# Kernel optimization log

Hardware: AMD Instinct MI355X
Metric: run time of the kernel (lower is better)

The kernel has to match this reference:

```python
import jax, jax.numpy as jnp
import numpy as np
import math

NUM_HEADS = 8
DIM_EMBED = 640
DIM_CROSS = 768
DIM_HEAD = DIM_EMBED // NUM_HEADS


def setup_inputs() -> dict:
    key = jax.random.key(0)
    ks = jax.random.split(key, 10)
    B, SQ, SKV = 32, 1024, 77
    s_e = 1.0 / math.sqrt(DIM_EMBED)
    s_c = 1.0 / math.sqrt(DIM_CROSS)
    return {
        "x": jax.random.normal(ks[0], (B, SQ, DIM_EMBED), jnp.float32),
        "y": jax.random.normal(ks[1], (B, SKV, DIM_CROSS), jnp.float32),
        "Wq": jax.random.normal(ks[2], (DIM_EMBED, DIM_EMBED), jnp.float32) * s_e,
        "bq": jax.random.normal(ks[3], (DIM_EMBED,), jnp.float32) * 0.01,
        "Wk": jax.random.normal(ks[4], (DIM_CROSS, DIM_EMBED), jnp.float32) * s_c,
        "bk": jax.random.normal(ks[5], (DIM_EMBED,), jnp.float32) * 0.01,
        "Wv": jax.random.normal(ks[6], (DIM_CROSS, DIM_EMBED), jnp.float32) * s_c,
        "bv": jax.random.normal(ks[7], (DIM_EMBED,), jnp.float32) * 0.01,
        "Wo": jax.random.normal(ks[8], (DIM_EMBED, DIM_EMBED), jnp.float32) * s_e,
        "bo": jax.random.normal(ks[9], (DIM_EMBED,), jnp.float32) * 0.01,
    }


def reference(x, y, Wq, bq, Wk, bk, Wv, bv, Wo, bo):
    B, SQ, E = x.shape
    H, D = NUM_HEADS, DIM_HEAD
    q = x @ Wq + bq                      # [B, SQ, E]
    k = y @ Wk + bk                      # [B, SKV, E]
    v = y @ Wv + bv                      # [B, SKV, E]
    q = q.reshape(B, SQ, H, D)
    k = k.reshape(B, -1, H, D)
    v = v.reshape(B, -1, H, D)
    scores = jnp.einsum("bqhd,bkhd->bhqk", q, k) / math.sqrt(D)
    w = jax.nn.softmax(scores, axis=-1)
    out = jnp.einsum("bhqk,bkhd->bqhd", w, v).reshape(B, SQ, E)
    return out @ Wo + bo
```

## Files before the change

kernel.cpp:

```cpp
#include <hip/hip_runtime.h>
#include <hip/hip_bf16.h>

typedef __bf16 bf16x8 __attribute__((ext_vector_type(8)));
typedef float f32x4 __attribute__((ext_vector_type(4)));
typedef unsigned short us8 __attribute__((ext_vector_type(8)));
typedef unsigned int u32x4 __attribute__((ext_vector_type(4)));

#define E_ 640
#define CD_ 768
#define B_ 32
#define SQ_ 1024
#define SKV_ 77
#define H_ 8
#define DH_ 80

typedef __attribute__((address_space(3))) unsigned int as3_u32;
typedef __attribute__((address_space(1))) const unsigned int as1_u32;

__device__ __forceinline__ void gload16(const unsigned short* g, unsigned short* l) {
    __builtin_amdgcn_global_load_lds((as1_u32*)g, (as3_u32*)l, 16, 0, 0);
}

__device__ __forceinline__ float b2f(unsigned short u) {
    unsigned int x = ((unsigned int)u) << 16;
    return __builtin_bit_cast(float, x);
}
__device__ __forceinline__ unsigned short f2b(float f) {
    unsigned int x = __builtin_bit_cast(unsigned int, f);
    x += 0x7fffu + ((x >> 16) & 1u);
    return (unsigned short)(x >> 16);
}
__device__ __forceinline__ bf16x8 lv8(const unsigned short* p) {
    return __builtin_bit_cast(bf16x8, *reinterpret_cast<const us8*>(p));
}
__device__ __forceinline__ bf16x8 zero8() {
    us8 z = {0,0,0,0,0,0,0,0};
    return __builtin_bit_cast(bf16x8, z);
}
__device__ __forceinline__ bf16x8 cvtpk8(f32x4 lo, f32x4 hi) {
    unsigned int w0, w1, w2, w3;
    asm("v_cvt_pk_bf16_f32 %0, %1, %2" : "=v"(w0) : "v"(lo[0]), "v"(lo[1]));
    asm("v_cvt_pk_bf16_f32 %0, %1, %2" : "=v"(w1) : "v"(lo[2]), "v"(lo[3]));
    asm("v_cvt_pk_bf16_f32 %0, %1, %2" : "=v"(w2) : "v"(hi[0]), "v"(hi[1]));
    asm("v_cvt_pk_bf16_f32 %0, %1, %2" : "=v"(w3) : "v"(hi[2]), "v"(hi[3]));
    u32x4 w = {w0, w1, w2, w3};
    return __builtin_bit_cast(bf16x8, w);
}
__device__ __forceinline__ us8 cvt8(const float* s) {
    f32x4 f0 = *reinterpret_cast<const f32x4*>(s);
    f32x4 f1 = *reinterpret_cast<const f32x4*>(s + 4);
    return __builtin_bit_cast(us8, cvtpk8(f0, f1));
}

__device__ __forceinline__ void transpose_body(
    const float* __restrict__ in, unsigned short* __restrict__ out,
    int K, int N, int bx, int by, unsigned short (*t)[33])
{
    const int tx = threadIdx.x & 31, ty = threadIdx.x >> 5;
    const int n0 = bx * 32, k0 = by * 32;
#pragma unroll
    for (int i = 0; i < 4; ++i)
        t[ty + 8*i][tx] = f2b(in[(size_t)(k0 + ty + 8*i) * N + n0 + tx]);
    __syncthreads();
#pragma unroll
    for (int i = 0; i < 4; ++i)
        out[(size_t)(n0 + ty + 8*i) * K + k0 + tx] = t[tx][ty + 8*i];
}

__global__ __launch_bounds__(256) void fused_prep(
    const float* __restrict__ Wq, unsigned short* __restrict__ WqT,
    const float* __restrict__ Wo, unsigned short* __restrict__ WoT,
    const float* __restrict__ Wk, unsigned short* __restrict__ WkT,
    const float* __restrict__ Wv, unsigned short* __restrict__ WvT,
    const float* __restrict__ x, unsigned short* __restrict__ Xb)
{
    __shared__ unsigned short t[32][33];
    const int id = blockIdx.x;
    if (id < 800) {
        int z = id / 400, rem = id % 400;
        transpose_body(z ? Wo : Wq, z ? WoT : WqT, 640, 640, rem % 20, rem / 20, t);
    } else if (id < 1760) {
        int id2 = id - 800, z = id2 / 480, rem = id2 % 480;
        transpose_body(z ? Wv : Wk, z ? WvT : WkT, 768, 640, rem % 20, rem / 20, t);
    } else {
        long i = (long)(id - 1760) * 256 + threadIdx.x;
        const long stride = 2048L * 256;
        for (const long n8 = 2621440L; i < n8; i += stride)
            *reinterpret_cast<us8*>(Xb + i * 8) = cvt8(x + i * 8);
    }
}

template<int AMODE, bool CF32>
__device__ __forceinline__ void gemm_body(
    const void* __restrict__ Ap,
    const unsigned short* __restrict__ Wt,
    const float* __restrict__ bias,
    void* __restrict__ Cp,
    int M, int K, int ldc, int m0, int n0,
    unsigned short* smem)
{
    const int tid = threadIdx.x, lane = tid & 63, wave = tid >> 6;
    const int wr = (wave >> 1) << 6, wc = (wave & 1) << 6;
    const int l15 = lane & 15, l4 = lane >> 4;
    const int sgz = (tid >> 3) & 3;
    const int srd = (l15 >> 1) & 3;
    const int rdo = (l4 ^ srd) << 3;

    const unsigned short* gW0 = Wt + (size_t)(n0 + (tid >> 2)) * K + (((tid & 3) ^ sgz) << 3);
    const unsigned short* gW1 = Wt + (size_t)(n0 + (tid >> 2) + 64) * K + (((tid & 3) ^ sgz) << 3);

    const unsigned short* gA0; const unsigned short* gA1;
    const float* fA0; const float* fA1;
    int sw0, sw1;
    if constexpr (AMODE == 0) {
        gA0 = (const unsigned short*)Ap + (size_t)(m0 + (tid >> 2)) * K + (((tid & 3) ^ sgz) << 3);
        gA1 = (const unsigned short*)Ap + (size_t)(m0 + (tid >> 2) + 64) * K + (((tid & 3) ^ sgz) << 3);
    } else {
        int r0 = m0 + (tid >> 2); if (r0 >= M) r0 = M - 1;
        int r1 = r0 + 64; if (r1 >= M) r1 = M - 1;
        fA0 = (const float*)Ap + (size_t)r0 * K + (tid & 3) * 8;
        fA1 = (const float*)Ap + (size_t)r1 * K + (tid & 3) * 8;
        sw0 = ((tid & ~3) | ((tid & 3) ^ sgz)) * 8;
        sw1 = sw0 + 256 * 8;
    }

    f32x4 acc[4][4];
#pragma unroll
    for (int m = 0; m < 4; ++m)
#pragma unroll
        for (int n = 0; n < 4; ++n)
#pragma unroll
            for (int i = 0; i < 4; ++i) acc[m][n][i] = 0.f;

    auto STAGE = [&](int buf) {
        unsigned short* As = smem + buf * 8192;
        unsigned short* Ws = As + 4096;
        if constexpr (AMODE == 0) {
            gload16(gA0, As + tid * 8);
            gload16(gA1, As + (tid + 256) * 8);
            gA0 += 32; gA1 += 32;
        } else {
            *reinterpret_cast<us8*>(As + sw0) = cvt8(fA0);
            *reinterpret_cast<us8*>(As + sw1) = cvt8(fA1);
            fA0 += 32; fA1 += 32;
        }
        gload16(gW0, Ws + tid * 8);
        gload16(gW1, Ws + (tid + 256) * 8);
        gW0 += 32; gW1 += 32;
    };
    auto COMPUTE = [&](int buf) {
        const unsigned short* As = smem + buf * 8192;
        const unsigned short* Ws = As + 4096;
        bf16x8 a[4], b[4];
#pragma unroll
        for (int m = 0; m < 4; ++m)
            a[m] = lv8(&As[(wr + m * 16 + l15) * 32 + rdo]);
#pragma unroll
        for (int n = 0; n < 4; ++n)
            b[n] = lv8(&Ws[(wc + n * 16 + l15) * 32 + rdo]);
        __builtin_amdgcn_s_setprio(1);
#pragma unroll
        for (int m = 0; m < 4; ++m)
#pragma unroll
            for (int n = 0; n < 4; ++n)
                acc[m][n] = __builtin_amdgcn_mfma_f32_16x16x32_bf16(a[m], b[n], acc[m][n], 0, 0, 0);
        __builtin_amdgcn_s_setprio(0);
    };

    const int nk = K >> 5;
    STAGE(0);
    __syncthreads();
    for (int kt = 0; kt < nk - 2; kt += 2) {
        STAGE(1);
        COMPUTE(0);
        __syncthreads();
        STAGE(0);
        COMPUTE(1);
        __syncthreads();
    }
    STAGE(1);
    COMPUTE(0);
    __syncthreads();
    COMPUTE(1);

    float bs[4];
#pragma unroll
    for (int n = 0; n < 4; ++n) bs[n] = bias[n0 + wc + n * 16 + l15];

    if constexpr (CF32) {
        float* C = (float*)Cp;
        float* fs = (float*)smem;
#pragma unroll
        for (int p = 0; p < 2; ++p) {
            __syncthreads();
            if (wr == p * 64) {
#pragma unroll
                for (int m = 0; m < 4; ++m)
#pragma unroll
                    for (int n = 0; n < 4; ++n)
#pragma unroll
                        for (int i = 0; i < 4; ++i)
                            fs[(m * 16 + l4 * 4 + i) * 128 + wc + n * 16 + l15] =
                                acc[m][n][i] + bs[n];
            }
            __syncthreads();
#pragma unroll
            for (int r = 0; r < 8; ++r) {
                const int off = (r * 256 + tid) * 4;
                const int row = off >> 7, col = off & 127;
                const int grow = m0 + p * 64 + row;
                if (grow < M)
                    *reinterpret_cast<f32x4*>(&C[(size_t)grow * ldc + n0 + col]) =
                        *reinterpret_cast<const f32x4*>(&fs[off]);
            }
        }
    } else {
        unsigned short* C = (unsigned short*)Cp;
#pragma unroll
        for (int p = 0; p < 2; ++p) {
            __syncthreads();
            if (wr == p * 64) {
#pragma unroll
                for (int m = 0; m < 4; ++m)
#pragma unroll
                    for (int n = 0; n < 4; ++n)
#pragma unroll
                        for (int i = 0; i < 4; ++i)
                            smem[(m * 16 + l4 * 4 + i) * 128 + wc + n * 16 + l15] =
                                f2b(acc[m][n][i] + bs[n]);
            }
            __syncthreads();
#pragma unroll
            for (int r = 0; r < 4; ++r) {
                const int off = (r * 256 + tid) * 8;
                const int row = off >> 7, col = off & 127;
                const int grow = m0 + p * 64 + row;
                if (grow < M)
                    *reinterpret_cast<us8*>(&C[(size_t)grow * ldc + n0 + col]) =
                        *reinterpret_cast<us8*>(&smem[off]);
            }
        }
    }
}

__global__ __launch_bounds__(256) void gemm_o(
    const unsigned short* __restrict__ Ap, const unsigned short* __restrict__ Wt,
    const float* __restrict__ bias, float* __restrict__ Cp)
{
    __shared__ __align__(16) unsigned short smem[16384];
    const int orig = blockIdx.x;
    const int wgid = (orig & 7) * 160 + (orig >> 3);
    gemm_body<0, true>(Ap, Wt, bias, Cp, 32768, 640, 640,
                       (wgid / 5) * 128, (wgid % 5) * 128, smem);
}

__global__ __launch_bounds__(256) void fused_qkv(
    const unsigned short* __restrict__ Xb, const unsigned short* __restrict__ WqT,
    const float* __restrict__ bq, unsigned short* __restrict__ Qb,
    const float* __restrict__ y,
    const unsigned short* __restrict__ WkT, const float* __restrict__ bk2, unsigned short* __restrict__ Kb,
    const unsigned short* __restrict__ WvT, const float* __restrict__ bv2, unsigned short* __restrict__ Vb)
{
    __shared__ __align__(16) unsigned short smem[16384];
    const int id = blockIdx.x;
    if (id < 200) {
        int z = id / 100, rem = id % 100;
        int m0 = (rem / 5) * 128, n0 = (rem % 5) * 128;
        if (z == 0) gemm_body<1, false>(y, WkT, bk2, Kb, 2464, 768, 640, m0, n0, smem);
        else        gemm_body<1, false>(y, WvT, bv2, Vb, 2464, 768, 640, m0, n0, smem);
    } else {
        int orig = id - 200;
        int wgid = (orig & 7) * 160 + (orig >> 3);
        int m0 = (wgid / 5) * 128, n0 = (wgid % 5) * 128;
        gemm_body<0, false>(Xb, WqT, bq, Qb, 32768, 640, 640, m0, n0, smem);
    }
}

__global__ __launch_bounds__(256) void vtrans_kernel(
    const unsigned short* __restrict__ Vb, unsigned short* __restrict__ Vt)
{
    __shared__ unsigned short Vl[77 * 88 + 8];
    const int b = blockIdx.x, h = blockIdx.y;
    const int tid = threadIdx.x;
    for (int idx = tid; idx < 770; idx += 256) {
        int kv = idx / 10, seg = idx % 10;
        *reinterpret_cast<us8*>(&Vl[kv * 88 + seg * 8]) =
            *reinterpret_cast<const us8*>(&Vb[(size_t)(b * 77 + kv) * 640 + h * 80 + seg * 8]);
    }
    __syncthreads();
    unsigned short* out = Vt + (size_t)(b * 8 + h) * 6400;
    for (int idx = tid; idx < 800; idx += 256) {
        int d = idx / 10, seg = idx % 10;
        us8 v;
#pragma unroll
        for (int j = 0; j < 8; ++j) {
            int kv = seg * 8 + j;
            v[j] = (kv < 77) ? Vl[kv * 88 + d] : (unsigned short)0;
        }
        *reinterpret_cast<us8*>(&out[d * 80 + seg * 8]) = v;
    }
}

__global__ __launch_bounds__(128) void attn_kernel(
    const unsigned short* __restrict__ Q,
    const unsigned short* __restrict__ Kp,
    const unsigned short* __restrict__ Vt,
    unsigned short* __restrict__ Oa)
{
    __shared__ __align__(16) unsigned short smem[11272];
    const int tid = threadIdx.x, lane = tid & 63, wave = tid >> 6;
    const int l15 = lane & 15, l4 = lane >> 4;
    const int qb = blockIdx.x * 128, h = blockIdx.y, b = blockIdx.z;
    const size_t qrow0 = (size_t)b * SQ_ + qb + wave * 64;
    const size_t kbase = (size_t)b * SKV_ * E_ + h * DH_;
    const size_t vbase = (size_t)(b * 8 + h) * 6400;

    bf16x8 aq[3][4];
#pragma unroll
    for (int ks = 0; ks < 3; ++ks) {
        const int d = ks * 32 + l4 * 8;
#pragma unroll
        for (int m = 0; m < 4; ++m)
            aq[ks][m] = (d < 80) ? lv8(&Q[(qrow0 + m * 16 + l15) * E_ + h * DH_ + d]) : zero8();
    }

    f32x4 accS[4][5];
#pragma unroll
    for (int m = 0; m < 4; ++m)
#pragma unroll
        for (int n = 0; n < 5; ++n)
#pragma unroll
            for (int i = 0; i < 4; ++i) accS[m][n][i] = 0.f;

#pragma unroll
    for (int ks = 0; ks < 3; ++ks) {
        const int d = ks * 32 + l4 * 8;
        bf16x8 bk[5];
#pragma unroll
        for (int n = 0; n < 5; ++n) {
            const int kv = n * 16 + l15;
            bk[n] = (kv < SKV_ && d < 80) ? lv8(&Kp[kbase + (size_t)kv * E_ + d]) : zero8();
        }
        __builtin_amdgcn_s_setprio(1);
#pragma unroll
        for (int n = 0; n < 5; ++n)
#pragma unroll
            for (int m = 0; m < 4; ++m)
                accS[m][n] = __builtin_amdgcn_mfma_f32_16x16x32_bf16(aq[ks][m], bk[n], accS[m][n], 0, 0, 0);
        __builtin_amdgcn_s_setprio(0);
    }

    unsigned short* Pw = smem + wave * 5632;

    const float scale = 0.11180339887498949f;
    float rs[4][4];
#pragma unroll
    for (int m = 0; m < 4; ++m) {
#pragma unroll
        for (int i = 0; i < 4; ++i) {
            float mx = -1e30f;
#pragma unroll
            for (int n = 0; n < 5; ++n) {
                float s = accS[m][n][i] * scale;
                if (n == 4 && l15 >= 13) s = -1e30f;
                accS[m][n][i] = s;
                mx = fmaxf(mx, s);
            }
            mx = fmaxf(mx, __shfl_xor(mx, 1));
            mx = fmaxf(mx, __shfl_xor(mx, 2));
            mx = fmaxf(mx, __shfl_xor(mx, 4));
            mx = fmaxf(mx, __shfl_xor(mx, 8));
            float sum = 0.f;
            const int prow = m * 16 + l4 * 4 + i;
#pragma unroll
            for (int n = 0; n < 5; ++n) {
                float p = __expf(accS[m][n][i] - mx);
                sum += p;
                Pw[prow * 88 + n * 16 + l15] = f2b(p);
            }
            sum += __shfl_xor(sum, 1);
            sum += __shfl_xor(sum, 2);
            sum += __shfl_xor(sum, 4);
            sum += __shfl_xor(sum, 8);
            rs[m][i] = sum;
        }
    }

    f32x4 accO[4][5];
#pragma unroll
    for (int m = 0; m < 4; ++m)
#pragma unroll
        for (int n = 0; n < 5; ++n)
#pragma unroll
            for (int i = 0; i < 4; ++i) accO[m][n][i] = 0.f;

#pragma unroll
    for (int ks = 0; ks < 3; ++ks) {
        const int kv = ks * 32 + l4 * 8;
        bf16x8 ap[4], bv[5];
#pragma unroll
        for (int m = 0; m < 4; ++m)
            ap[m] = (ks < 2 || l4 < 2) ? lv8(&Pw[(m * 16 + l15) * 88 + ks * 32 + l4 * 8])
                                       : zero8();
#pragma unroll
        for (int n = 0; n < 5; ++n) {
            const int d = n * 16 + l15;
            bv[n] = (kv < 80) ? lv8(&Vt[vbase + (size_t)d * 80 + kv]) : zero8();
        }
        __builtin_amdgcn_s_setprio(1);
#pragma unroll
        for (int n = 0; n < 5; ++n)
#pragma unroll
            for (int m = 0; m < 4; ++m)
                accO[m][n] = __builtin_amdgcn_mfma_f32_16x16x32_bf16(ap[m], bv[n], accO[m][n], 0, 0, 0);
        __builtin_amdgcn_s_setprio(0);
    }

    __syncthreads();
#pragma unroll
    for (int m = 0; m < 4; ++m) {
#pragma unroll
        for (int i = 0; i < 4; ++i) {
            const float inv = 1.f / rs[m][i];
            const int rl = wave * 64 + m * 16 + l4 * 4 + i;
#pragma unroll
            for (int n = 0; n < 5; ++n)
                smem[rl * 80 + n * 16 + l15] = f2b(accO[m][n][i] * inv);
        }
    }
    __syncthreads();
    const size_t obase = (size_t)b * SQ_ + qb;
    for (int idx = tid; idx < 1280; idx += 128) {
        int row = idx / 10, seg = idx % 10;
        *reinterpret_cast<us8*>(&Oa[(obase + row) * E_ + h * DH_ + seg * 8]) =
            *reinterpret_cast<us8*>(&smem[row * 80 + seg * 8]);
    }
}

extern "C" void kernel_launch(void* const* d_in, const int* in_sizes, int n_in,
                              void* d_out, int out_size, void* d_ws, size_t ws_size,
                              hipStream_t stream) {
    const float* x  = (const float*)d_in[0];
    const float* y  = (const float*)d_in[1];
    const float* Wq = (const float*)d_in[2];
    const float* bq = (const float*)d_in[3];
    const float* Wk = (const float*)d_in[4];
    const float* bk = (const float*)d_in[5];
    const float* Wv = (const float*)d_in[6];
    const float* bv = (const float*)d_in[7];
    const float* Wo = (const float*)d_in[8];
    const float* bo = (const float*)d_in[9];
    float* out = (float*)d_out;

    char* ws = (char*)d_ws;
    unsigned short* WqT = (unsigned short*)(ws + 0);
    unsigned short* WkT = (unsigned short*)(ws + 819200);
    unsigned short* WvT = (unsigned short*)(ws + 1802240);
    unsigned short* WoT = (unsigned short*)(ws + 2785280);
    unsigned short* Qb  = (unsigned short*)(ws + 3604480);
    unsigned short* Kb  = (unsigned short*)(ws + 45547520);
    unsigned short* Vb  = (unsigned short*)(ws + 48701440);
    unsigned short* Xb  = (unsigned short*)(ws + 51855360);
    unsigned short* Vtb = (unsigned short*)(ws + 51855360);

    fused_prep<<<3808, 256, 0, stream>>>(Wq, WqT, Wo, WoT, Wk, WkT, Wv, WvT, x, Xb);
    fused_qkv<<<1480, 256, 0, stream>>>(Xb, WqT, bq, Qb, y, WkT, bk, Kb, WvT, bv, Vb);
    vtrans_kernel<<<dim3(32, 8), 256, 0, stream>>>(Vb, Vtb);
    attn_kernel<<<dim3(8, 8, 32), 128, 0, stream>>>(Qb, Kb, Vtb, Qb);
    gemm_o<<<1280, 256, 0, stream>>>(Qb, WoT, bo, out);
}
```

Baseline: 172.5 us.

## Rebalance kernel stages: fuse x conversion with K/V GEMMs and V transpose with Q GEMM

Moves the x-to-bf16 conversion out of the weight-prep kernel into the K/V projection kernel, and folds the standalone V transpose into the Q projection kernel as extra blocks. This cuts one kernel launch and lets the small K/V GEMM and V transpose work overlap with larger, bandwidth-bound work instead of running as separate, underfilled stages. Vt now gets its own workspace region instead of aliasing Xb, because Xb is still being read while the transpose runs.

```diff
diff --git a/kernel.cpp b/kernel.cpp
--- a/kernel.cpp
+++ b/kernel.cpp
@@ -71,22 +71,16 @@
     const float* __restrict__ Wq, unsigned short* __restrict__ WqT,
     const float* __restrict__ Wo, unsigned short* __restrict__ WoT,
     const float* __restrict__ Wk, unsigned short* __restrict__ WkT,
-    const float* __restrict__ Wv, unsigned short* __restrict__ WvT,
-    const float* __restrict__ x, unsigned short* __restrict__ Xb)
+    const float* __restrict__ Wv, unsigned short* __restrict__ WvT)
 {
     __shared__ unsigned short t[32][33];
     const int id = blockIdx.x;
     if (id < 800) {
         int z = id / 400, rem = id % 400;
         transpose_body(z ? Wo : Wq, z ? WoT : WqT, 640, 640, rem % 20, rem / 20, t);
-    } else if (id < 1760) {
+    } else {
         int id2 = id - 800, z = id2 / 480, rem = id2 % 480;
         transpose_body(z ? Wv : Wk, z ? WvT : WkT, 768, 640, rem % 20, rem / 20, t);
-    } else {
-        long i = (long)(id - 1760) * 256 + threadIdx.x;
-        const long stride = 2048L * 256;
-        for (const long n8 = 2621440L; i < n8; i += stride)
-            *reinterpret_cast<us8*>(Xb + i * 8) = cvt8(x + i * 8);
     }
 }
 
@@ -243,20 +237,8 @@
     }
 }
 
-__global__ __launch_bounds__(256) void gemm_o(
-    const unsigned short* __restrict__ Ap, const unsigned short* __restrict__ Wt,
-    const float* __restrict__ bias, float* __restrict__ Cp)
-{
-    __shared__ __align__(16) unsigned short smem[16384];
-    const int orig = blockIdx.x;
-    const int wgid = (orig & 7) * 160 + (orig >> 3);
-    gemm_body<0, true>(Ap, Wt, bias, Cp, 32768, 640, 640,
-                       (wgid / 5) * 128, (wgid % 5) * 128, smem);
-}
-
-__global__ __launch_bounds__(256) void fused_qkv(
-    const unsigned short* __restrict__ Xb, const unsigned short* __restrict__ WqT,
-    const float* __restrict__ bq, unsigned short* __restrict__ Qb,
+__global__ __launch_bounds__(256) void fused_cvt_kv(
+    const float* __restrict__ x, unsigned short* __restrict__ Xb,
     const float* __restrict__ y,
     const unsigned short* __restrict__ WkT, const float* __restrict__ bk2, unsigned short* __restrict__ Kb,
     const unsigned short* __restrict__ WvT, const float* __restrict__ bv2, unsigned short* __restrict__ Vb)
@@ -269,18 +251,17 @@
         if (z == 0) gemm_body<1, false>(y, WkT, bk2, Kb, 2464, 768, 640, m0, n0, smem);
         else        gemm_body<1, false>(y, WvT, bv2, Vb, 2464, 768, 640, m0, n0, smem);
     } else {
-        int orig = id - 200;
-        int wgid = (orig & 7) * 160 + (orig >> 3);
-        int m0 = (wgid / 5) * 128, n0 = (wgid % 5) * 128;
-        gemm_body<0, false>(Xb, WqT, bq, Qb, 32768, 640, 640, m0, n0, smem);
-    }
-}
-
-__global__ __launch_bounds__(256) void vtrans_kernel(
-    const unsigned short* __restrict__ Vb, unsigned short* __restrict__ Vt)
-{
-    __shared__ unsigned short Vl[77 * 88 + 8];
-    const int b = blockIdx.x, h = blockIdx.y;
+        long i = (long)(id - 200) * 256 + threadIdx.x;
+        const long stride = 2048L * 256;
+        for (const long n8 = 2621440L; i < n8; i += stride)
+            *reinterpret_cast<us8*>(Xb + i * 8) = cvt8(x + i * 8);
+    }
+}
+
+__device__ __forceinline__ void vtrans_body(
+    const unsigned short* __restrict__ Vb, unsigned short* __restrict__ Vt,
+    int b, int h, unsigned short* Vl)
+{
     const int tid = threadIdx.x;
     for (int idx = tid; idx < 770; idx += 256) {
         int kv = idx / 10, seg = idx % 10;
@@ -299,6 +280,34 @@
         }
         *reinterpret_cast<us8*>(&out[d * 80 + seg * 8]) = v;
     }
+}
+
+__global__ __launch_bounds__(256) void fused_q_vt(
+    const unsigned short* __restrict__ Xb, const unsigned short* __restrict__ WqT,
+    const float* __restrict__ bq, unsigned short* __restrict__ Qb,
+    const unsigned short* __restrict__ Vb, unsigned short* __restrict__ Vtb)
+{
+    __shared__ __align__(16) unsigned short smem[16384];
+    const int id = blockIdx.x;
+    if (id < 1280) {
+        int wgid = (id & 7) * 160 + (id >> 3);
+        int m0 = (wgid / 5) * 128, n0 = (wgid % 5) * 128;
+        gemm_body<0, false>(Xb, WqT, bq, Qb, 32768, 640, 640, m0, n0, smem);
+    } else {
+        int r = id - 1280;
+        vtrans_body(Vb, Vtb, r >> 3, r & 7, smem);
+    }
+}
+
+__global__ __launch_bounds__(256) void gemm_o(
+    const unsigned short* __restrict__ Ap, const unsigned short* __restrict__ Wt,
+    const float* __restrict__ bias, float* __restrict__ Cp)
+{
+    __shared__ __align__(16) unsigned short smem[16384];
+    const int orig = blockIdx.x;
+    const int wgid = (orig & 7) * 160 + (orig >> 3);
+    gemm_body<0, true>(Ap, Wt, bias, Cp, 32768, 640, 640,
+                       (wgid / 5) * 128, (wgid % 5) * 128, smem);
 }
 
 __global__ __launch_bounds__(128) void attn_kernel(
@@ -461,11 +470,11 @@
     unsigned short* Kb  = (unsigned short*)(ws + 45547520);
     unsigned short* Vb  = (unsigned short*)(ws + 48701440);
     unsigned short* Xb  = (unsigned short*)(ws + 51855360);
-    unsigned short* Vtb = (unsigned short*)(ws + 51855360);
-
-    fused_prep<<<3808, 256, 0, stream>>>(Wq, WqT, Wo, WoT, Wk, WkT, Wv, WvT, x, Xb);
-    fused_qkv<<<1480, 256, 0, stream>>>(Xb, WqT, bq, Qb, y, WkT, bk, Kb, WvT, bv, Vb);
-    vtrans_kernel<<<dim3(32, 8), 256, 0, stream>>>(Vb, Vtb);
+    unsigned short* Vtb = (unsigned short*)(ws + 93798400);
+
+    fused_prep<<<1760, 256, 0, stream>>>(Wq, WqT, Wo, WoT, Wk, WkT, Wv, WvT);
+    fused_cvt_kv<<<2248, 256, 0, stream>>>(x, Xb, y, WkT, bk, Kb, WvT, bv, Vb);
+    fused_q_vt<<<1536, 256, 0, stream>>>(Xb, WqT, bq, Qb, Vb, Vtb);
     attn_kernel<<<dim3(8, 8, 32), 128, 0, stream>>>(Qb, Kb, Vtb, Qb);
     gemm_o<<<1280, 256, 0, stream>>>(Qb, WoT, bo, out);
 }
```

New measurement: 177.2 us. 1.03x slower.

## Triple-buffer GEMM pipeline with vmcnt waits and pre-convert y to bf16

Applied to the files above, without the earlier changes.

Replaces the double-buffered GEMM main loop with a three-stage ring buffer. It prefetches two K-tiles ahead, waits on vmcnt counters and issues a single barrier per iteration instead of two. The K/V projection previously converted y from fp32 inline; y is now converted to bf16 in the prep kernel so every GEMM uses async global-to-LDS loads. LDS use per block rises to 48KB, which may lower occupancy, and Yb reuses the Vt buffer region.

```diff
diff --git a/kernel.cpp b/kernel.cpp
--- a/kernel.cpp
+++ b/kernel.cpp
@@ -72,7 +72,8 @@
     const float* __restrict__ Wo, unsigned short* __restrict__ WoT,
     const float* __restrict__ Wk, unsigned short* __restrict__ WkT,
     const float* __restrict__ Wv, unsigned short* __restrict__ WvT,
-    const float* __restrict__ x, unsigned short* __restrict__ Xb)
+    const float* __restrict__ x, unsigned short* __restrict__ Xb,
+    const float* __restrict__ y, unsigned short* __restrict__ Yb)
 {
     __shared__ unsigned short t[32][33];
     const int id = blockIdx.x;
@@ -82,17 +83,22 @@
     } else if (id < 1760) {
         int id2 = id - 800, z = id2 / 480, rem = id2 % 480;
         transpose_body(z ? Wv : Wk, z ? WvT : WkT, 768, 640, rem % 20, rem / 20, t);
-    } else {
+    } else if (id < 3808) {
         long i = (long)(id - 1760) * 256 + threadIdx.x;
         const long stride = 2048L * 256;
         for (const long n8 = 2621440L; i < n8; i += stride)
             *reinterpret_cast<us8*>(Xb + i * 8) = cvt8(x + i * 8);
-    }
-}
-
-template<int AMODE, bool CF32>
-__device__ __forceinline__ void gemm_body(
-    const void* __restrict__ Ap,
+    } else {
+        long i = (long)(id - 3808) * 256 + threadIdx.x;
+        const long stride = 240L * 256;
+        for (const long n8 = 236544L; i < n8; i += stride)
+            *reinterpret_cast<us8*>(Yb + i * 8) = cvt8(y + i * 8);
+    }
+}
+
+template<bool CF32>
+__device__ __forceinline__ void gemm_pipe(
+    const unsigned short* __restrict__ A,
     const unsigned short* __restrict__ Wt,
     const float* __restrict__ bias,
     void* __restrict__ Cp,
@@ -108,21 +114,8 @@
 
     const unsigned short* gW0 = Wt + (size_t)(n0 + (tid >> 2)) * K + (((tid & 3) ^ sgz) << 3);
     const unsigned short* gW1 = Wt + (size_t)(n0 + (tid >> 2) + 64) * K + (((tid & 3) ^ sgz) << 3);
-
-    const unsigned short* gA0; const unsigned short* gA1;
-    const float* fA0; const float* fA1;
-    int sw0, sw1;
-    if constexpr (AMODE == 0) {
-        gA0 = (const unsigned short*)Ap + (size_t)(m0 + (tid >> 2)) * K + (((tid & 3) ^ sgz) << 3);
-        gA1 = (const unsigned short*)Ap + (size_t)(m0 + (tid >> 2) + 64) * K + (((tid & 3) ^ sgz) << 3);
-    } else {
-        int r0 = m0 + (tid >> 2); if (r0 >= M) r0 = M - 1;
-        int r1 = r0 + 64; if (r1 >= M) r1 = M - 1;
-        fA0 = (const float*)Ap + (size_t)r0 * K + (tid & 3) * 8;
-        fA1 = (const float*)Ap + (size_t)r1 * K + (tid & 3) * 8;
-        sw0 = ((tid & ~3) | ((tid & 3) ^ sgz)) * 8;
-        sw1 = sw0 + 256 * 8;
-    }
+    const unsigned short* gA0 = A + (size_t)(m0 + (tid >> 2)) * K + (((tid & 3) ^ sgz) << 3);
+    const unsigned short* gA1 = A + (size_t)(m0 + (tid >> 2) + 64) * K + (((tid & 3) ^ sgz) << 3);
 
     f32x4 acc[4][4];
 #pragma unroll
@@ -135,18 +128,11 @@
     auto STAGE = [&](int buf) {
         unsigned short* As = smem + buf * 8192;
         unsigned short* Ws = As + 4096;
-        if constexpr (AMODE == 0) {
-            gload16(gA0, As + tid * 8);
-            gload16(gA1, As + (tid + 256) * 8);
-            gA0 += 32; gA1 += 32;
-        } else {
-            *reinterpret_cast<us8*>(As + sw0) = cvt8(fA0);
-            *reinterpret_cast<us8*>(As + sw1) = cvt8(fA1);
-            fA0 += 32; fA1 += 32;
-        }
+        gload16(gA0, As + tid * 8);
+        gload16(gA1, As + (tid + 256) * 8);
         gload16(gW0, Ws + tid * 8);
         gload16(gW1, Ws + (tid + 256) * 8);
-        gW0 += 32; gW1 += 32;
+        gA0 += 32; gA1 += 32; gW0 += 32; gW1 += 32;
     };
     auto COMPUTE = [&](int buf) {
         const unsigned short* As = smem + buf * 8192;
@@ -169,19 +155,15 @@
 
     const int nk = K >> 5;
     STAGE(0);
-    __syncthreads();
-    for (int kt = 0; kt < nk - 2; kt += 2) {
-        STAGE(1);
-        COMPUTE(0);
-        __syncthreads();
-        STAGE(0);
-        COMPUTE(1);
-        __syncthreads();
-    }
     STAGE(1);
-    COMPUTE(0);
-    __syncthreads();
-    COMPUTE(1);
+    for (int t = 0; t < nk; ++t) {
+        if (t == nk - 1) { asm volatile("s_waitcnt vmcnt(0)" ::: "memory"); }
+        else             { asm volatile("s_waitcnt vmcnt(4)" ::: "memory"); }
+        __builtin_amdgcn_sched_barrier(0);
+        __builtin_amdgcn_s_barrier();
+        COMPUTE(t % 3);
+        if (t + 2 < nk) STAGE((t + 2) % 3);
+    }
 
     float bs[4];
 #pragma unroll
@@ -243,36 +225,25 @@
     }
 }
 
-__global__ __launch_bounds__(256) void gemm_o(
-    const unsigned short* __restrict__ Ap, const unsigned short* __restrict__ Wt,
-    const float* __restrict__ bias, float* __restrict__ Cp)
-{
-    __shared__ __align__(16) unsigned short smem[16384];
-    const int orig = blockIdx.x;
-    const int wgid = (orig & 7) * 160 + (orig >> 3);
-    gemm_body<0, true>(Ap, Wt, bias, Cp, 32768, 640, 640,
-                       (wgid / 5) * 128, (wgid % 5) * 128, smem);
-}
-
 __global__ __launch_bounds__(256) void fused_qkv(
     const unsigned short* __restrict__ Xb, const unsigned short* __restrict__ WqT,
     const float* __restrict__ bq, unsigned short* __restrict__ Qb,
-    const float* __restrict__ y,
+    const unsigned short* __restrict__ Yb,
     const unsigned short* __restrict__ WkT, const float* __restrict__ bk2, unsigned short* __restrict__ Kb,
     const unsigned short* __restrict__ WvT, const float* __restrict__ bv2, unsigned short* __restrict__ Vb)
 {
-    __shared__ __align__(16) unsigned short smem[16384];
+    __shared__ __align__(16) unsigned short smem[24576];
     const int id = blockIdx.x;
     if (id < 200) {
         int z = id / 100, rem = id % 100;
         int m0 = (rem / 5) * 128, n0 = (rem % 5) * 128;
-        if (z == 0) gemm_body<1, false>(y, WkT, bk2, Kb, 2464, 768, 640, m0, n0, smem);
-        else        gemm_body<1, false>(y, WvT, bv2, Vb, 2464, 768, 640, m0, n0, smem);
+        if (z == 0) gemm_pipe<false>(Yb, WkT, bk2, Kb, 2464, 768, 640, m0, n0, smem);
+        else        gemm_pipe<false>(Yb, WvT, bv2, Vb, 2464, 768, 640, m0, n0, smem);
     } else {
         int orig = id - 200;
         int wgid = (orig & 7) * 160 + (orig >> 3);
         int m0 = (wgid / 5) * 128, n0 = (wgid % 5) * 128;
-        gemm_body<0, false>(Xb, WqT, bq, Qb, 32768, 640, 640, m0, n0, smem);
+        gemm_pipe<false>(Xb, WqT, bq, Qb, 32768, 640, 640, m0, n0, smem);
     }
 }
 
@@ -280,7 +251,7 @@
     const unsigned short* __restrict__ Vb, unsigned short* __restrict__ Vt)
 {
     __shared__ unsigned short Vl[77 * 88 + 8];
-    const int b = blockIdx.x, h = blockIdx.y;
+    const int r = blockIdx.x, b = r >> 3, h = r & 7;
     const int tid = threadIdx.x;
     for (int idx = tid; idx < 770; idx += 256) {
         int kv = idx / 10, seg = idx % 10;
@@ -299,6 +270,17 @@
         }
         *reinterpret_cast<us8*>(&out[d * 80 + seg * 8]) = v;
     }
+}
+
+__global__ __launch_bounds__(256) void gemm_o(
+    const unsigned short* __restrict__ Ap, const unsigned short* __restrict__ Wt,
+    const float* __restrict__ bias, float* __restrict__ Cp)
+{
+    __shared__ __align__(16) unsigned short smem[24576];
+    const int orig = blockIdx.x;
+    const int wgid = (orig & 7) * 160 + (orig >> 3);
+    gemm_pipe<true>(Ap, Wt, bias, Cp, 32768, 640, 640,
+                    (wgid / 5) * 128, (wgid % 5) * 128, smem);
 }
 
 __global__ __launch_bounds__(128) void attn_kernel(
@@ -461,11 +443,12 @@
     unsigned short* Kb  = (unsigned short*)(ws + 45547520);
     unsigned short* Vb  = (unsigned short*)(ws + 48701440);
     unsigned short* Xb  = (unsigned short*)(ws + 51855360);
-    unsigned short* Vtb = (unsigned short*)(ws + 51855360);
-
-    fused_prep<<<3808, 256, 0, stream>>>(Wq, WqT, Wo, WoT, Wk, WkT, Wv, WvT, x, Xb);
-    fused_qkv<<<1480, 256, 0, stream>>>(Xb, WqT, bq, Qb, y, WkT, bk, Kb, WvT, bv, Vb);
-    vtrans_kernel<<<dim3(32, 8), 256, 0, stream>>>(Vb, Vtb);
+    unsigned short* Vtb = (unsigned short*)(ws + 93798400);
+    unsigned short* Yb  = Vtb;
+
+    fused_prep<<<4048, 256, 0, stream>>>(Wq, WqT, Wo, WoT, Wk, WkT, Wv, WvT, x, Xb, y, Yb);
+    fused_qkv<<<1480, 256, 0, stream>>>(Xb, WqT, bq, Qb, Yb, WkT, bk, Kb, WvT, bv, Vb);
+    vtrans_kernel<<<256, 256, 0, stream>>>(Vb, Vtb);
     attn_kernel<<<dim3(8, 8, 32), 128, 0, stream>>>(Qb, Kb, Vtb, Qb);
     gemm_o<<<1280, 256, 0, stream>>>(Qb, WoT, bo, out);
 }
```

New measurement: 155.8 us. 9.7% less time.
